# Performance work log

Hardware: AMD Instinct MI355X
Metric: run time of the kernel (lower is better)

## Reference

```python
import jax, jax.numpy as jnp
import numpy as np
import math

N = 8192
NFEAT = 63
NHID = 1024
NLAYERS = 7
LAMBDA = 1.5
ALPHA = 0.7
NEG = -1e12


def setup_inputs() -> dict:
    key = jax.random.key(0)
    ks = jax.random.split(key, 12)
    x = jax.random.normal(ks[0], (N, NFEAT), dtype=jnp.float32)
    # dist acts as a (normalized) propagation matrix; scale by 1/N for numerical stability
    dist = jax.random.uniform(ks[1], (N, N), dtype=jnp.float32) / N
    adj = jax.random.randint(ks[2], (N, N), 0, 2, dtype=jnp.int32)
    # parameters
    fc_W = jax.random.normal(ks[3], (NFEAT, NHID), dtype=jnp.float32) * 0.1
    fc_b = jnp.zeros((NHID,), dtype=jnp.float32)
    stdv = 1.0 / math.sqrt(NHID)
    conv_W = jax.random.uniform(ks[4], (NLAYERS, NHID, NHID), dtype=jnp.float32,
                                minval=-stdv, maxval=stdv)
    gat_W = jax.random.normal(ks[5], (NHID, NHID), dtype=jnp.float32) * (1.414 / math.sqrt(NHID))
    gat_a = jax.random.normal(ks[6], (2 * NHID, 1), dtype=jnp.float32) * 0.05
    cls1_W = jax.random.normal(ks[7], (NHID, 64), dtype=jnp.float32) * (1.0 / math.sqrt(NHID))
    cls1_b = jnp.zeros((64,), dtype=jnp.float32)
    cls3_W = jax.random.normal(ks[8], (64, 1), dtype=jnp.float32) * 0.125
    cls3_b = jnp.zeros((1,), dtype=jnp.float32)
    return {"x": x, "dist": dist, "adj": adj, "fc_W": fc_W, "fc_b": fc_b,
            "conv_W": conv_W, "gat_W": gat_W, "gat_a": gat_a,
            "cls1_W": cls1_W, "cls1_b": cls1_b, "cls3_W": cls3_W, "cls3_b": cls3_b}


def _theta(l):
    return min(1.0, math.log(LAMBDA / l + 1.0))


def reference(x, dist, adj, fc_W, fc_b, conv_W, gat_W, gat_a, cls1_W, cls1_b, cls3_W, cls3_b):
    # eval mode: all dropouts are identity
    h = jax.nn.relu(x @ fc_W + fc_b)          # [N, H]
    h0 = h
    # GCNII-style propagation layers
    for i in range(NLAYERS):
        theta = _theta(i + 1)
        hi = dist @ h                          # [N, H] sparse-style propagation
        support = (1.0 - ALPHA) * hi + ALPHA * h0
        out = theta * (support @ conv_W[i]) + (1.0 - theta) * support + h
        h = jax.nn.relu(out)
    # GAT layer (l = 9). Faithful math, but computed without the N*N*2F tensor:
    # e_ij = leakyrelu(h_i' @ a1 + h_j' @ a2) with h' = h @ W
    hp = h @ gat_W                             # [N, H]
    a1 = gat_a[:NHID, 0]                       # [H]
    a2 = gat_a[NHID:, 0]                       # [H]
    e = jax.nn.leaky_relu(hp @ a1[:, None] + (hp @ a2[:, None]).T, negative_slope=0.2)  # [N, N]
    e = jnp.where(adj > 0, e, NEG)
    attention = jax.nn.softmax(e, axis=1)      # [N, N]
    theta = _theta(9)
    hi = attention @ h                         # note: attends over layer input h, not hp
    support = (1.0 - ALPHA) * hi + ALPHA * h0
    out = theta * (support @ gat_W) + (1.0 - theta) * support + h
    h = jax.nn.elu(out)
    h = jax.nn.relu(h @ cls1_W + cls1_b)
    out = jax.nn.sigmoid(h @ cls3_W + cls3_b)  # [N, 1]
    return out.squeeze(-1)                     # [N]
```

## Files before the change

kernel.cpp:

```cpp
#include <hip/hip_runtime.h>
#include <math.h>

#define NN 8192
#define NH 1024

typedef __bf16 bf16x8 __attribute__((ext_vector_type(8)));
typedef float floatx4 __attribute__((ext_vector_type(4)));
typedef unsigned short us8 __attribute__((ext_vector_type(8)));
typedef unsigned short us;

__device__ __forceinline__ unsigned short f2bf(float f) {
  unsigned int u = __float_as_uint(f);
  u += 0x7fffu + ((u >> 16) & 1u);
  return (unsigned short)(u >> 16);
}

__device__ __forceinline__ void async16(const void* g, void* l) {
  __builtin_amdgcn_global_load_lds(
      (__attribute__((address_space(1))) void*)(g),
      (__attribute__((address_space(3))) void*)(l), 16, 0, 0);
}

__global__ __launch_bounds__(512, 2)
void gemm_big(const us* __restrict__ A, const us* __restrict__ Bt,
              const float* __restrict__ aux, float* __restrict__ supf,
              us* __restrict__ supb)
{
  __shared__ __align__(16) us lsm[73728];
  us* lB = lsm;
  us* lA = lsm + 24576;

  const int id = blockIdx.x;
  const int yt = id & 31;
  const int xt = id >> 5;

  const int tid  = threadIdx.x;
  const int lane = tid & 63;
  const int wave = tid >> 6;
  const long tileM = (long)yt * 256;
  const long tileN = (long)xt * 128;
  const int wm = (wave & 3) * 64;
  const int wn = (wave >> 2) * 64;

  const int chunk8 = (tid & 7) ^ ((tid >> 3) & 7);
  const us* gA0 = A + (tileM + (tid >> 3)) * 8192L + chunk8 * 8;
  const us* gB0 = Bt + (tileN + (tid >> 3)) * 8192L + chunk8 * 8;
  const int lo = tid * 8;

  const int fr = lane & 15;
  const int q  = lane >> 4;
  const int cx0 = ((q) ^ (fr & 7)) * 8;
  const int cx1 = ((4 + q) ^ (fr & 7)) * 8;

  floatx4 zero4 = {0.f, 0.f, 0.f, 0.f};
  floatx4 acc[4][4];
#pragma unroll
  for (int i = 0; i < 4; ++i)
#pragma unroll
    for (int j = 0; j < 4; ++j) acc[i][j] = zero4;

#define STAGE_BIG(s, kf)                                                  \
  {                                                                       \
    const long ko = (long)(kf) << 6;                                      \
    async16(gA0 + ko,              lA + (s)*16384 + lo);                  \
    async16(gA0 + 64 * 8192L + ko, lA + (s)*16384 + 4096 + lo);           \
    async16(gA0 + 128 * 8192L + ko, lA + (s)*16384 + 8192 + lo);          \
    async16(gA0 + 192 * 8192L + ko, lA + (s)*16384 + 12288 + lo);         \
    async16(gB0 + ko,              lB + (s)*8192 + lo);                   \
    async16(gB0 + 64 * 8192L + ko, lB + (s)*8192 + 4096 + lo);            \
  }

#define KSTEP_BIG(s, kf)                                                  \
  {                                                                       \
    asm volatile("s_waitcnt vmcnt(6)\n\ts_barrier" ::: "memory");         \
    STAGE_BIG((((s) + 2) % 3), kf);                                       \
    bf16x8 af[2][4], bfr[2][4];                                           \
    _Pragma("unroll") for (int i = 0; i < 4; ++i) {                       \
      af[0][i] = *(const bf16x8*)&lA[(s)*16384 + (wm + 16 * i + fr) * 64 + cx0]; \
      af[1][i] = *(const bf16x8*)&lA[(s)*16384 + (wm + 16 * i + fr) * 64 + cx1]; \
    }                                                                     \
    _Pragma("unroll") for (int j = 0; j < 4; ++j) {                       \
      bfr[0][j] = *(const bf16x8*)&lB[(s)*8192 + (wn + 16 * j + fr) * 64 + cx0]; \
      bfr[1][j] = *(const bf16x8*)&lB[(s)*8192 + (wn + 16 * j + fr) * 64 + cx1]; \
    }                                                                     \
    _Pragma("unroll") for (int kk = 0; kk < 2; ++kk)                      \
      _Pragma("unroll") for (int i = 0; i < 4; ++i)                       \
        _Pragma("unroll") for (int j = 0; j < 4; ++j)                     \
            acc[i][j] = __builtin_amdgcn_mfma_f32_16x16x32_bf16(          \
                af[kk][i], bfr[kk][j], acc[i][j], 0, 0, 0);               \
  }

  STAGE_BIG(0, 0)
  STAGE_BIG(1, 1)

  for (int kt = 0; kt < 126; kt += 3) {
    KSTEP_BIG(0, kt + 2)
    KSTEP_BIG(1, kt + 3)
    KSTEP_BIG(2, kt + 4)
  }
  KSTEP_BIG(0, 127)
  KSTEP_BIG(1, 127)
  asm volatile("s_waitcnt vmcnt(0)" ::: "memory");

  const int crow = (lane >> 4) * 4;
#pragma unroll
  for (int i = 0; i < 4; ++i)
#pragma unroll
    for (int j = 0; j < 4; ++j)
#pragma unroll
      for (int r = 0; r < 4; ++r) {
        long row = tileM + wm + 16 * i + crow + r;
        long col = tileN + wn + 16 * j + fr;
        long idx = row * NH + col;
        float s = 0.3f * acc[i][j][r] + 0.7f * aux[idx];
        supf[idx] = s;
        supb[idx] = f2bf(s);
      }
#undef STAGE_BIG
#undef KSTEP_BIG
}

template<int EPI>
__global__ __launch_bounds__(256)
void gemm_db(const us* __restrict__ A, const us* __restrict__ Bt, int K,
             const float* __restrict__ aux, float* __restrict__ iof,
             us* __restrict__ outb, us* __restrict__ hTb, float theta)
{
  __shared__ __align__(16) us lsm[32768];
  us* lB = lsm;
  us* lA = lsm + 16384;

  const int id = blockIdx.x;
  const int xcd = id & 7, slot = id >> 3;
  const int xt = slot & 7;
  const int yt = xcd + 8 * (slot >> 3);

  const int tid  = threadIdx.x;
  const int lane = tid & 63;
  const int wave = tid >> 6;
  const long tileM = (long)yt * 128;
  const long tileN = (long)xt * 128;
  const int wm = (wave & 1) * 64;
  const int wn = (wave >> 1) * 64;

  const int chunk = (tid & 3) ^ ((tid >> 3) & 3);
  const us* gA0 = A + (tileM + (tid >> 2)) * (long)K + chunk * 8;
  const us* gA1 = gA0 + 64L * K;
  const us* gB0 = Bt + (tileN + (tid >> 2)) * (long)K + chunk * 8;
  const us* gB1 = gB0 + 64L * K;
  const int lo = tid * 8;

  const int fr = lane & 15;
  const int q8 = (lane >> 4) * 8;
  const int q8x = q8 ^ ((fr & 6) << 2);

  floatx4 zero4 = {0.f, 0.f, 0.f, 0.f};
  floatx4 acc[4][4];
#pragma unroll
  for (int i = 0; i < 4; ++i)
#pragma unroll
    for (int j = 0; j < 4; ++j) acc[i][j] = zero4;

#define STAGE_DB(s, kf)                                                   \
  {                                                                       \
    const int k0 = (kf) << 5;                                             \
    async16(gA0 + k0, lA + (s)*4096 + lo);                                \
    async16(gA1 + k0, lA + (s)*4096 + 2048 + lo);                         \
    async16(gB0 + k0, lB + (s)*4096 + lo);                                \
    async16(gB1 + k0, lB + (s)*4096 + 2048 + lo);                        \
  }

#define KSTEP_DB(s, kf)                                                   \
  {                                                                       \
    asm volatile("s_waitcnt vmcnt(8)\n\ts_barrier" ::: "memory");         \
    STAGE_DB((((s) + 3) & 3), kf);                                        \
    bf16x8 af[4], bfr[4];                                                 \
    _Pragma("unroll") for (int i = 0; i < 4; ++i)                         \
        af[i] = *(const bf16x8*)&lA[(s)*4096 + (wm + 16 * i + fr) * 32 + q8x]; \
    _Pragma("unroll") for (int j = 0; j < 4; ++j)                         \
        bfr[j] = *(const bf16x8*)&lB[(s)*4096 + (wn + 16 * j + fr) * 32 + q8x]; \
    _Pragma("unroll") for (int i = 0; i < 4; ++i)                         \
        _Pragma("unroll") for (int j = 0; j < 4; ++j)                     \
            acc[i][j] = __builtin_amdgcn_mfma_f32_16x16x32_bf16(          \
                af[i], bfr[j], acc[i][j], 0, 0, 0);                       \
  }

  STAGE_DB(0, 0)
  STAGE_DB(1, 1)
  STAGE_DB(2, 2)

  for (int kt = 0; kt < 32; kt += 4) {
    int k3 = kt + 3; if (k3 > 31) k3 = 31;
    int k4 = kt + 4; if (k4 > 31) k4 = 31;
    int k5 = kt + 5; if (k5 > 31) k5 = 31;
    int k6 = kt + 6; if (k6 > 31) k6 = 31;
    KSTEP_DB(0, k3)
    KSTEP_DB(1, k4)
    KSTEP_DB(2, k5)
    KSTEP_DB(3, k6)
  }
  asm volatile("s_waitcnt vmcnt(0)" ::: "memory");
  __syncthreads();

  us* ldsT = lsm;
  const int crow = (lane >> 4) * 4;
#pragma unroll
  for (int i = 0; i < 4; ++i) {
#pragma unroll
    for (int j = 0; j < 4; ++j) {
#pragma unroll
      for (int r = 0; r < 4; ++r) {
        int lr = wm + 16 * i + crow + r;
        int lc = wn + 16 * j + fr;
        long idx = (tileM + lr) * NH + tileN + lc;
        float o = theta * acc[i][j][r] + (1.f - theta) * aux[idx] + iof[idx];
        o = (EPI == 1) ? fmaxf(o, 0.f) : (o > 0.f ? o : __expf(o) - 1.f);
        iof[idx] = o;
        if (EPI == 1) ldsT[lc * 136 + lr] = f2bf(o);
        if (EPI == 2) outb[idx] = f2bf(o);
      }
    }
  }
  if (EPI == 1) {
    __syncthreads();
    int ch = tid & 15;
    int c0 = tid >> 4;
#pragma unroll
    for (int it = 0; it < 8; ++it) {
      int c = c0 + it * 16;
      us8 v = *(const us8*)&ldsT[c * 136 + ch * 8];
      *(us8*)&hTb[(tileN + c) * 8192L + tileM + ch * 8] = v;
    }
  }
#undef STAGE_DB
#undef KSTEP_DB
}

__global__ __launch_bounds__(256)
void cls_gemm(const us* __restrict__ hb, const us* __restrict__ W1t,
              const float* __restrict__ b1, const float* __restrict__ W3,
              const float* __restrict__ b3, float* __restrict__ out)
{
  __shared__ __align__(16) us lA[4096];
  __shared__ __align__(16) us lB[2048];
  const int tid = threadIdx.x, lane = tid & 63, wave = tid >> 6;
  const long tileM = (long)blockIdx.x * 128;
  const us* gA0 = hb + (tileM + (tid >> 2)) * 1024L + (tid & 3) * 8;
  const us* gA1 = gA0 + 64 * 1024L;
  const us* gB0 = W1t + (tid >> 2) * 1024L + (tid & 3) * 8;
  const int fr = lane & 15, q8 = (lane >> 4) * 8;
  const int wm = wave * 32;

  floatx4 zero4 = {0.f, 0.f, 0.f, 0.f};
  floatx4 acc[2][4];
#pragma unroll
  for (int i = 0; i < 2; ++i)
#pragma unroll
    for (int j = 0; j < 4; ++j) acc[i][j] = zero4;

  for (int kt = 0; kt < 32; ++kt) {
    const int k0 = kt << 5;
    async16(gA0 + k0, lA + tid * 8);
    async16(gA1 + k0, lA + 2048 + tid * 8);
    async16(gB0 + k0, lB + tid * 8);
    __syncthreads();
    bf16x8 af[2], bfr[4];
#pragma unroll
    for (int i = 0; i < 2; ++i)
      af[i] = *(const bf16x8*)&lA[(wm + 16 * i + fr) * 32 + q8];
#pragma unroll
    for (int j = 0; j < 4; ++j)
      bfr[j] = *(const bf16x8*)&lB[(16 * j + fr) * 32 + q8];
#pragma unroll
    for (int i = 0; i < 2; ++i)
#pragma unroll
      for (int j = 0; j < 4; ++j)
        acc[i][j] = __builtin_amdgcn_mfma_f32_16x16x32_bf16(af[i], bfr[j], acc[i][j], 0, 0, 0);
    __syncthreads();
  }

  float b1v[4], w3v[4];
#pragma unroll
  for (int j = 0; j < 4; ++j) { b1v[j] = b1[16 * j + fr]; w3v[j] = W3[16 * j + fr]; }
  const float b3v = b3[0];
  const int crow = (lane >> 4) * 4;
#pragma unroll
  for (int i = 0; i < 2; ++i)
#pragma unroll
    for (int r = 0; r < 4; ++r) {
      float v = 0.f;
#pragma unroll
      for (int j = 0; j < 4; ++j)
        v += fmaxf(acc[i][j][r] + b1v[j], 0.f) * w3v[j];
      v += __shfl_xor(v, 1);
      v += __shfl_xor(v, 2);
      v += __shfl_xor(v, 4);
      v += __shfl_xor(v, 8);
      if (fr == 0)
        out[tileM + wm + 16 * i + crow + r] = 1.f / (1.f + __expf(-(v + b3v)));
    }
}

__global__ __launch_bounds__(256)
void transpose_f32_bf16(const float* __restrict__ src, us* __restrict__ dst,
                        int R, int C) {
  __shared__ float t[32][33];
  int tid = threadIdx.x;
  int tx = tid & 31, ty = tid >> 5;
  long r0 = (long)blockIdx.y * 32, c0 = (long)blockIdx.x * 32;
#pragma unroll
  for (int i = 0; i < 32; i += 8)
    t[ty + i][tx] = src[(r0 + ty + i) * C + c0 + tx];
  __syncthreads();
#pragma unroll
  for (int i = 0; i < 32; i += 8)
    dst[(c0 + ty + i) * R + r0 + tx] = f2bf(t[tx][ty + i]);
}

__global__ __launch_bounds__(256)
void f32_to_bf16_vec(const float* __restrict__ s, us* __restrict__ d) {
  long i = (blockIdx.x * 256L + threadIdx.x) * 4;
  float4 v = *(const float4*)(s + i);
  *(ushort4*)(d + i) = make_ushort4(f2bf(v.x), f2bf(v.y), f2bf(v.z), f2bf(v.w));
}

__global__ __launch_bounds__(256)
void fc_kernel(const float* __restrict__ x, const float* __restrict__ W,
               const float* __restrict__ b, float* __restrict__ h0f,
               float* __restrict__ hf) {
  __shared__ float xs[64];
  int row = blockIdx.x, tid = threadIdx.x;
  if (tid < 63) xs[tid] = x[row * 63 + tid];
  __syncthreads();
#pragma unroll
  for (int q = 0; q < 4; ++q) {
    int c = tid + q * 256;
    float s = b[c];
    for (int k = 0; k < 63; ++k) s += xs[k] * W[k * NH + c];
    s = fmaxf(s, 0.f);
    long idx = (long)row * NH + c;
    h0f[idx] = s;
    hf[idx] = s;
  }
}

__global__ __launch_bounds__(256)
void wv_kernel(const float* __restrict__ W, const float* __restrict__ a,
               float* __restrict__ va1, float* __restrict__ va2) {
  int k = blockIdx.x, tid = threadIdx.x;
  float s1 = 0.f, s2 = 0.f;
  for (int n = tid; n < NH; n += 256) {
    float w = W[(long)k * NH + n];
    s1 += w * a[n];
    s2 += w * a[NH + n];
  }
#pragma unroll
  for (int o = 32; o; o >>= 1) { s1 += __shfl_down(s1, o); s2 += __shfl_down(s2, o); }
  __shared__ float r1[4], r2[4];
  int wave = tid >> 6;
  if ((tid & 63) == 0) { r1[wave] = s1; r2[wave] = s2; }
  __syncthreads();
  if (tid == 0) {
    va1[k] = r1[0] + r1[1] + r1[2] + r1[3];
    va2[k] = r2[0] + r2[1] + r2[2] + r2[3];
  }
}

__global__ __launch_bounds__(256)
void fg_kernel(const float* __restrict__ h, const float* __restrict__ va1,
               const float* __restrict__ va2, float* __restrict__ fv,
               float* __restrict__ gv) {
  int row = blockIdx.x, tid = threadIdx.x;
  float s1 = 0.f, s2 = 0.f;
  for (int k = tid; k < NH; k += 256) {
    float v = h[(long)row * NH + k];
    s1 += v * va1[k];
    s2 += v * va2[k];
  }
#pragma unroll
  for (int o = 32; o; o >>= 1) { s1 += __shfl_down(s1, o); s2 += __shfl_down(s2, o); }
  __shared__ float r1[4], r2[4];
  int wave = tid >> 6;
  if ((tid & 63) == 0) { r1[wave] = s1; r2[wave] = s2; }
  __syncthreads();
  if (tid == 0) {
    fv[row] = r1[0] + r1[1] + r1[2] + r1[3];
    gv[row] = r2[0] + r2[1] + r2[2] + r2[3];
  }
}

__global__ __launch_bounds__(256)
void attn_fused(const int* __restrict__ adj, const float* __restrict__ f,
                const float* __restrict__ g, us* __restrict__ P) {
  const int row = blockIdx.x, tid = threadIdx.x;
  const float fi = f[row];
  const int4* arow = (const int4*)(adj + (long)row * NN);
  float m = -3.0e38f, s = 0.f;
  for (int c = tid; c < NN / 4; c += 256) {
    int4 a = arow[c];
    float4 gg = *(const float4*)(g + c * 4);
#pragma unroll
    for (int t = 0; t < 4; ++t) {
      int av = (t == 0) ? a.x : (t == 1) ? a.y : (t == 2) ? a.z : a.w;
      float gvv = (t == 0) ? gg.x : (t == 1) ? gg.y : (t == 2) ? gg.z : gg.w;
      if (av > 0) {
        float e = fi + gvv;
        e = e > 0.f ? e : 0.2f * e;
        if (e > m) { s = s * __expf(m - e) + 1.f; m = e; }
        else s += __expf(e - m);
      }
    }
  }
#pragma unroll
  for (int o = 32; o; o >>= 1) {
    float m2 = __shfl_down(m, o), s2 = __shfl_down(s, o);
    float mn = fmaxf(m, m2);
    s = s * __expf(m - mn) + s2 * __expf(m2 - mn);
    m = mn;
  }
  __shared__ float ms[4], ss[4], bcast[2];
  int wave = tid >> 6;
  if ((tid & 63) == 0) { ms[wave] = m; ss[wave] = s; }
  __syncthreads();
  if (tid == 0) {
    float mm = ms[0], sv = ss[0];
    for (int w = 1; w < 4; ++w) {
      float mn = fmaxf(mm, ms[w]);
      sv = sv * __expf(mm - mn) + ss[w] * __expf(ms[w] - mn);
      mm = mn;
    }
    bcast[0] = mm;
    bcast[1] = sv;
  }
  __syncthreads();
  const float M = bcast[0], L = bcast[1];
  const bool uni = !(L > 0.f);
  const float inv = uni ? 0.f : 1.f / L;
  for (int c = tid; c < NN / 4; c += 256) {
    int4 a = arow[c];
    float4 gg = *(const float4*)(g + c * 4);
    float p[4];
#pragma unroll
    for (int t = 0; t < 4; ++t) {
      int av = (t == 0) ? a.x : (t == 1) ? a.y : (t == 2) ? a.z : a.w;
      float gvv = (t == 0) ? gg.x : (t == 1) ? gg.y : (t == 2) ? gg.z : gg.w;
      float e = fi + gvv;
      e = e > 0.f ? e : 0.2f * e;
      float pv = (av > 0) ? __expf(e - M) * inv : 0.f;
      if (uni) pv = 1.f / (float)NN;
      p[t] = pv;
    }
    *(ushort4*)(P + ((long)row << 13) + c * 4) =
        make_ushort4(f2bf(p[0]), f2bf(p[1]), f2bf(p[2]), f2bf(p[3]));
  }
}

extern "C" void kernel_launch(void* const* d_in, const int* in_sizes, int n_in,
                              void* d_out, int out_size, void* d_ws, size_t ws_size,
                              hipStream_t stream) {
  const float* x      = (const float*)d_in[0];
  const float* dist   = (const float*)d_in[1];
  const int*   adj    = (const int*)d_in[2];
  const float* fc_W   = (const float*)d_in[3];
  const float* fc_b   = (const float*)d_in[4];
  const float* conv_W = (const float*)d_in[5];
  const float* gat_W  = (const float*)d_in[6];
  const float* gat_a  = (const float*)d_in[7];
  const float* cls1_W = (const float*)d_in[8];
  const float* cls1_b = (const float*)d_in[9];
  const float* cls3_W = (const float*)d_in[10];
  const float* cls3_b = (const float*)d_in[11];
  float* out = (float*)d_out;

  char* p = (char*)d_ws;
  auto alloc = [&](size_t bytes) {
    char* r = p;
    p += (bytes + 255) & ~(size_t)255;
    return r;
  };
  us* distb   = (us*)alloc((size_t)NN * NN * 2);
  float* h0f  = (float*)alloc((size_t)NN * NH * 4);
  float* hf   = (float*)alloc((size_t)NN * NH * 4);
  float* supf = (float*)alloc((size_t)NN * NH * 4);
  us* supb    = (us*)alloc((size_t)NN * NH * 2);
  us* hb      = (us*)alloc((size_t)NN * NH * 2);
  us* hTb     = (us*)alloc((size_t)NN * NH * 2);
  us* convWT  = (us*)alloc((size_t)7 * NH * NH * 2);
  us* gatWT   = (us*)alloc((size_t)NH * NH * 2);
  us* W1t     = (us*)alloc((size_t)64 * NH * 2);
  float* va1 = (float*)alloc(NH * 4);
  float* va2 = (float*)alloc(NH * 4);
  float* fv  = (float*)alloc(NN * 4);
  float* gv  = (float*)alloc(NN * 4);

  float th[7];
  for (int l = 0; l < 7; ++l) {
    float t = logf(1.5f / (float)(l + 1) + 1.f);
    th[l] = t < 1.f ? t : 1.f;
  }
  float th9 = logf(1.5f / 9.f + 1.f);

  f32_to_bf16_vec<<<(NN * (long)NN) / (4 * 256), 256, 0, stream>>>(dist, distb);
  for (int i = 0; i < 7; ++i)
    transpose_f32_bf16<<<dim3(32, 32), 256, 0, stream>>>(
        conv_W + (size_t)i * NH * NH, convWT + (size_t)i * NH * NH, NH, NH);
  transpose_f32_bf16<<<dim3(32, 32), 256, 0, stream>>>(gat_W, gatWT, NH, NH);
  transpose_f32_bf16<<<dim3(2, 32), 256, 0, stream>>>(cls1_W, W1t, NH, 64);

  fc_kernel<<<NN, 256, 0, stream>>>(x, fc_W, fc_b, h0f, hf);
  transpose_f32_bf16<<<dim3(NH / 32, NN / 32), 256, 0, stream>>>(hf, hTb, NN, NH);

  for (int l = 0; l < 7; ++l) {
    gemm_big<<<256, 512, 0, stream>>>(distb, hTb, h0f, supf, supb);
    gemm_db<1><<<512, 256, 0, stream>>>(supb, convWT + (size_t)l * NH * NH, NH,
                                        supf, hf, nullptr, hTb, th[l]);
  }

  wv_kernel<<<NH, 256, 0, stream>>>(gat_W, gat_a, va1, va2);
  fg_kernel<<<NN, 256, 0, stream>>>(hf, va1, va2, fv, gv);
  attn_fused<<<NN, 256, 0, stream>>>(adj, fv, gv, distb);

  gemm_big<<<256, 512, 0, stream>>>(distb, hTb, h0f, supf, supb);
  gemm_db<2><<<512, 256, 0, stream>>>(supb, gatWT, NH, supf, hf, hb, nullptr, th9);

  cls_gemm<<<64, 256, 0, stream>>>(hb, W1t, cls1_b, cls3_W, cls3_b, out);
}
```

Before: 2.178 ms.

## Split big GEMM k-step into two phases with ping-pong barriers and MFMA priority

Restructures the main propagation GEMM's k-loop so each 64-wide k tile is processed in two half-phases. Each phase loads half the fragments, syncs, and issues 16 MFMAs under raised wave priority with sched_barrier fences. The async global-to-LDS prefetch for the next stage moves into the second phase, after its LDS reads are issued. The aim is to interleave LDS reads, global prefetch and MFMA across the two waves per SIMD (ping-pong scheduling), at the cost of an extra barrier per k step.

```diff
diff --git a/kernel.cpp b/kernel.cpp
--- a/kernel.cpp
+++ b/kernel.cpp
@@ -62,44 +62,63 @@
 #define STAGE_BIG(s, kf)                                                  \
   {                                                                       \
     const long ko = (long)(kf) << 6;                                      \
-    async16(gA0 + ko,              lA + (s)*16384 + lo);                  \
-    async16(gA0 + 64 * 8192L + ko, lA + (s)*16384 + 4096 + lo);           \
+    async16(gA0 + ko,               lA + (s)*16384 + lo);                 \
+    async16(gA0 + 64 * 8192L + ko,  lA + (s)*16384 + 4096 + lo);          \
     async16(gA0 + 128 * 8192L + ko, lA + (s)*16384 + 8192 + lo);          \
     async16(gA0 + 192 * 8192L + ko, lA + (s)*16384 + 12288 + lo);         \
-    async16(gB0 + ko,              lB + (s)*8192 + lo);                   \
-    async16(gB0 + 64 * 8192L + ko, lB + (s)*8192 + 4096 + lo);            \
-  }
-
-#define KSTEP_BIG(s, kf)                                                  \
-  {                                                                       \
-    asm volatile("s_waitcnt vmcnt(6)\n\ts_barrier" ::: "memory");         \
-    STAGE_BIG((((s) + 2) % 3), kf);                                       \
-    bf16x8 af[2][4], bfr[2][4];                                           \
-    _Pragma("unroll") for (int i = 0; i < 4; ++i) {                       \
-      af[0][i] = *(const bf16x8*)&lA[(s)*16384 + (wm + 16 * i + fr) * 64 + cx0]; \
-      af[1][i] = *(const bf16x8*)&lA[(s)*16384 + (wm + 16 * i + fr) * 64 + cx1]; \
-    }                                                                     \
-    _Pragma("unroll") for (int j = 0; j < 4; ++j) {                       \
-      bfr[0][j] = *(const bf16x8*)&lB[(s)*8192 + (wn + 16 * j + fr) * 64 + cx0]; \
-      bfr[1][j] = *(const bf16x8*)&lB[(s)*8192 + (wn + 16 * j + fr) * 64 + cx1]; \
-    }                                                                     \
-    _Pragma("unroll") for (int kk = 0; kk < 2; ++kk)                      \
-      _Pragma("unroll") for (int i = 0; i < 4; ++i)                       \
+    async16(gB0 + ko,               lB + (s)*8192 + lo);                  \
+    async16(gB0 + 64 * 8192L + ko,  lB + (s)*8192 + 4096 + lo);           \
+  }
+
+#define MFMA16(af, bfr)                                                   \
+    __builtin_amdgcn_s_setprio(1);                                        \
+    _Pragma("unroll") for (int i = 0; i < 4; ++i)                         \
         _Pragma("unroll") for (int j = 0; j < 4; ++j)                     \
             acc[i][j] = __builtin_amdgcn_mfma_f32_16x16x32_bf16(          \
-                af[kk][i], bfr[kk][j], acc[i][j], 0, 0, 0);               \
+                af[i], bfr[j], acc[i][j], 0, 0, 0);                       \
+    __builtin_amdgcn_s_setprio(0);                                        \
+    __builtin_amdgcn_sched_barrier(0);
+
+#define PHASE_A(s)                                                        \
+  {                                                                       \
+    bf16x8 af[4], bfr[4];                                                 \
+    _Pragma("unroll") for (int i = 0; i < 4; ++i)                         \
+      af[i] = *(const bf16x8*)&lA[(s)*16384 + (wm + 16 * i + fr) * 64 + cx0]; \
+    _Pragma("unroll") for (int j = 0; j < 4; ++j)                         \
+      bfr[j] = *(const bf16x8*)&lB[(s)*8192 + (wn + 16 * j + fr) * 64 + cx0]; \
+    __builtin_amdgcn_s_barrier();                                         \
+    asm volatile("s_waitcnt lgkmcnt(0)" ::: "memory");                    \
+    __builtin_amdgcn_sched_barrier(0);                                    \
+    MFMA16(af, bfr)                                                       \
+  }
+
+#define PHASE_B(s, kf)                                                    \
+  {                                                                       \
+    bf16x8 af[4], bfr[4];                                                 \
+    _Pragma("unroll") for (int i = 0; i < 4; ++i)                         \
+      af[i] = *(const bf16x8*)&lA[(s)*16384 + (wm + 16 * i + fr) * 64 + cx1]; \
+    _Pragma("unroll") for (int j = 0; j < 4; ++j)                         \
+      bfr[j] = *(const bf16x8*)&lB[(s)*8192 + (wn + 16 * j + fr) * 64 + cx1]; \
+    STAGE_BIG((((s) + 2) % 3), kf);                                       \
+    asm volatile("s_waitcnt vmcnt(6)" ::: "memory");                      \
+    __builtin_amdgcn_s_barrier();                                         \
+    asm volatile("s_waitcnt lgkmcnt(0)" ::: "memory");                    \
+    __builtin_amdgcn_sched_barrier(0);                                    \
+    MFMA16(af, bfr)                                                       \
   }
 
   STAGE_BIG(0, 0)
   STAGE_BIG(1, 1)
+  asm volatile("s_waitcnt vmcnt(6)" ::: "memory");
+  __builtin_amdgcn_s_barrier();
 
   for (int kt = 0; kt < 126; kt += 3) {
-    KSTEP_BIG(0, kt + 2)
-    KSTEP_BIG(1, kt + 3)
-    KSTEP_BIG(2, kt + 4)
-  }
-  KSTEP_BIG(0, 127)
-  KSTEP_BIG(1, 127)
+    PHASE_A(0) PHASE_B(0, kt + 2)
+    PHASE_A(1) PHASE_B(1, kt + 3)
+    PHASE_A(2) PHASE_B(2, kt + 4)
+  }
+  PHASE_A(0) PHASE_B(0, 127)
+  PHASE_A(1) PHASE_B(1, 127)
   asm volatile("s_waitcnt vmcnt(0)" ::: "memory");
 
   const int crow = (lane >> 4) * 4;
@@ -117,7 +136,9 @@
         supb[idx] = f2bf(s);
       }
 #undef STAGE_BIG
-#undef KSTEP_BIG
+#undef MFMA16
+#undef PHASE_A
+#undef PHASE_B
 }
 
 template<int EPI>
@@ -167,7 +188,7 @@
     async16(gA0 + k0, lA + (s)*4096 + lo);                                \
     async16(gA1 + k0, lA + (s)*4096 + 2048 + lo);                         \
     async16(gB0 + k0, lB + (s)*4096 + lo);                                \
-    async16(gB1 + k0, lB + (s)*4096 + 2048 + lo);                        \
+    async16(gB1 + k0, lB + (s)*4096 + 2048 + lo);                         \
   }
 
 #define KSTEP_DB(s, kf)                                                   \
```

Result: no change. 2.192 ms (+0.6%).
